# Performance work log

Measured on AMD Instinct MI355X. Metric: run time of the kernel, lower is better.

Reference implementation:

```python
import jax, jax.numpy as jnp
import numpy as np

HEADS = 8
HID = 128
N_A = 10000
N_B = 10000
E = 120000
NG = 8  # graphs in batch
F_A = 256
F_B = 128
NEG_SLOPE = 0.2


def _gat(h_src, h_dst, src, dst, ws, wd, a_s, a_d, bias, num_dst):
    """PyG GATConv, bipartite, concat=False, add_self_loops=False."""
    hs = (h_src @ ws).reshape(-1, HEADS, HID)   # [N_src, H, C]
    hd = (h_dst @ wd).reshape(-1, HEADS, HID)   # [N_dst, H, C]
    al_s = jnp.sum(hs * a_s, axis=-1)           # [N_src, H]
    al_d = jnp.sum(hd * a_d, axis=-1)           # [N_dst, H]
    e = jax.nn.leaky_relu(al_s[src] + al_d[dst], NEG_SLOPE)  # [E, H]
    m = jax.ops.segment_max(e, dst, num_segments=num_dst)
    ex = jnp.exp(e - m[dst])
    denom = jax.ops.segment_sum(ex, dst, num_segments=num_dst)
    alpha = ex / (denom[dst] + 1e-16)           # segment softmax over in-edges
    msg = hs[src] * alpha[:, :, None]           # [E, H, C]
    out = jax.ops.segment_sum(msg, dst, num_segments=num_dst)
    return out.mean(axis=1) + bias              # concat=False -> head mean + bias


def _mean_pool(x, batch, num_graphs):
    s = jax.ops.segment_sum(x, batch, num_segments=num_graphs)
    cnt = jax.ops.segment_sum(jnp.ones((x.shape[0],), x.dtype), batch, num_segments=num_graphs)
    return s / jnp.maximum(cnt, 1.0)[:, None]


def setup_inputs() -> dict:
    key = jax.random.key(0)
    ks = iter(jax.random.split(key, 48))
    rn = lambda shape, s=0.05: jax.random.normal(next(ks), shape, jnp.float32) * s
    inp = {
        'x_a': jax.random.normal(next(ks), (N_A, F_A), jnp.float32),
        'x_b': jax.random.normal(next(ks), (N_B, F_B), jnp.float32),
        'edge_ab': jax.random.randint(next(ks), (2, E), 0, N_A, jnp.int32),
        'edge_ba': jax.random.randint(next(ks), (2, E), 0, N_B, jnp.int32),
        'batch_a': jnp.sort(jax.random.randint(next(ks), (N_A,), 0, NG, jnp.int32)),
        'batch_b': jnp.sort(jax.random.randint(next(ks), (N_B,), 0, NG, jnp.int32)),
        'lin_a_w': rn((F_A, HID)), 'lin_a_b': rn((HID,)),
        'lin_b_w': rn((F_B, HID)), 'lin_b_b': rn((HID,)),
        'fc_w': rn((2 * HID, 1)), 'fc_b': rn((1,)),
    }
    for layer in ('1', '2'):
        for rel in ('ab', 'ba'):
            inp[f'w{layer}s_{rel}'] = rn((HID, HEADS * HID))
            inp[f'w{layer}d_{rel}'] = rn((HID, HEADS * HID))
            inp[f'a{layer}s_{rel}'] = rn((HEADS, HID))
            inp[f'a{layer}d_{rel}'] = rn((HEADS, HID))
            inp[f'b{layer}_{rel}'] = rn((HID,))
    return inp


def reference(x_a, x_b, edge_ab, edge_ba, batch_a, batch_b,
              lin_a_w, lin_a_b, lin_b_w, lin_b_b, fc_w, fc_b,
              w1s_ab, w1d_ab, a1s_ab, a1d_ab, b1_ab,
              w1s_ba, w1d_ba, a1s_ba, a1d_ba, b1_ba,
              w2s_ab, w2d_ab, a2s_ab, a2d_ab, b2_ab,
              w2s_ba, w2d_ba, a2s_ba, a2d_ba, b2_ba):
    ha = jax.nn.relu(x_a @ lin_a_w + lin_a_b)
    hb = jax.nn.relu(x_b @ lin_b_w + lin_b_b)
    # layer 1 (each dst type receives exactly one relation -> HeteroConv mean is identity)
    hb1 = _gat(ha, hb, edge_ab[0], edge_ab[1], w1s_ab, w1d_ab, a1s_ab, a1d_ab, b1_ab, N_B)
    ha1 = _gat(hb, ha, edge_ba[0], edge_ba[1], w1s_ba, w1d_ba, a1s_ba, a1d_ba, b1_ba, N_A)
    ha1 = jax.nn.relu(ha1)
    hb1 = jax.nn.relu(hb1)
    # layer 2
    hb2 = _gat(ha1, hb1, edge_ab[0], edge_ab[1], w2s_ab, w2d_ab, a2s_ab, a2d_ab, b2_ab, N_B)
    ha2 = _gat(hb1, ha1, edge_ba[0], edge_ba[1], w2s_ba, w2d_ba, a2s_ba, a2d_ba, b2_ba, N_A)
    pa = _mean_pool(ha2, batch_a, NG)
    pb = _mean_pool(hb2, batch_b, NG)
    g = jnp.concatenate([pa, pb], axis=1)       # [NG, 2*HID]
    return (g @ fc_w + fc_b).squeeze(-1)        # [NG]
```

## Files before the change

### kernel.cpp

```cpp
#include <hip/hip_runtime.h>
#include <math.h>

#define HID 128
#define HEADS 8

typedef __attribute__((ext_vector_type(8))) short s16x8;
typedef __attribute__((ext_vector_type(4))) float f32x4;

__device__ __forceinline__ unsigned short bf16_rne(float x) {
  unsigned u = __float_as_uint(x);
  unsigned r = u + 0x7FFFu + ((u >> 16) & 1u);
  return (unsigned short)(r >> 16);
}
__device__ __forceinline__ float bf16f(unsigned short h) {
  return __uint_as_float(((unsigned)h) << 16);
}

struct PrepArgs {
  const float* W[8];
  const float* a[8];
  unsigned short* WThi[4];
  unsigned short* WTlo[4];
  float* v[8];
};
struct PrepX {
  const float* lwa; const float* lwb;
  unsigned short *wa_hi, *wa_lo, *wb_hi, *wb_lo;
  int KA, KB, nta, ntb;
};

__global__ __launch_bounds__(256) void prep_hist(
    PrepArgs p, PrepX px,
    const int* __restrict__ dst_ab, const int* __restrict__ dst_ba,
    int* __restrict__ cnt_ab, int* __restrict__ cnt_ba, int E)
{
  __shared__ float tile[64][65];
  const int bid = blockIdx.x;
  const int tid = threadIdx.x;
  const int a = tid >> 2;
  const int cg = (tid & 3) << 4;

  if (bid < 128) {
    const int g = bid >> 5;
    const int rem = bid & 31;
    const int h = rem >> 2;
    const int t = rem & 3;
    const int k0 = (t >> 1) << 6, c0 = (t & 1) << 6;
    const float* src = p.W[2 * g] + (size_t)(k0 + a) * 1024 + h * 128 + c0 + cg;
#pragma unroll
    for (int i = 0; i < 16; i += 4) {
      const float4 v4 = *(const float4*)(src + i);
      tile[a][cg + i + 0] = v4.x; tile[a][cg + i + 1] = v4.y;
      tile[a][cg + i + 2] = v4.z; tile[a][cg + i + 3] = v4.w;
    }
    __syncthreads();
    const size_t ob = (size_t)(c0 + a) * 1024 + h * 128 + k0 + cg;
    unsigned hw[8], lw_[8];
#pragma unroll
    for (int i = 0; i < 8; i++) {
      float x0 = tile[cg + 2 * i][a];
      float x1 = tile[cg + 2 * i + 1][a];
      unsigned short h0 = bf16_rne(x0), h1 = bf16_rne(x1);
      unsigned short l0 = bf16_rne(x0 - bf16f(h0)), l1 = bf16_rne(x1 - bf16f(h1));
      hw[i]  = (unsigned)h0 | ((unsigned)h1 << 16);
      lw_[i] = (unsigned)l0 | ((unsigned)l1 << 16);
    }
    *(uint4*)(p.WThi[g] + ob)     = make_uint4(hw[0], hw[1], hw[2], hw[3]);
    *(uint4*)(p.WThi[g] + ob + 8) = make_uint4(hw[4], hw[5], hw[6], hw[7]);
    *(uint4*)(p.WTlo[g] + ob)     = make_uint4(lw_[0], lw_[1], lw_[2], lw_[3]);
    *(uint4*)(p.WTlo[g] + ob + 8) = make_uint4(lw_[4], lw_[5], lw_[6], lw_[7]);
  } else if (bid < 160) {
    const int u = bid - 128;
    const int wi = u >> 2;
    const int gid = ((u & 3) << 8) + tid;
    const int k = gid >> 3, h = gid & 7;
    const float* wr = p.W[wi] + (size_t)k * (HEADS * HID) + h * HID;
    const float* ar = p.a[wi] + (size_t)h * HID;
    float s = 0.f;
    for (int c = 0; c < HID; c++) s = fmaf(wr[c], ar[c], s);
    p.v[wi][gid] = s;
  } else if (bid < 160 + px.nta + px.ntb) {
    const bool isa = (bid - 160) < px.nta;
    const int b = isa ? (bid - 160) : (bid - 160 - px.nta);
    const int K = isa ? px.KA : px.KB;
    const float* lw = isa ? px.lwa : px.lwb;
    unsigned short* ohi = isa ? px.wa_hi : px.wb_hi;
    unsigned short* olo = isa ? px.wa_lo : px.wb_lo;
    const int k0 = (b >> 1) << 6, c0 = (b & 1) << 6;
    const float* src = lw + (size_t)(k0 + a) * 128 + c0 + cg;
#pragma unroll
    for (int i = 0; i < 16; i += 4) {
      const float4 v4 = *(const float4*)(src + i);
      tile[a][cg + i + 0] = v4.x; tile[a][cg + i + 1] = v4.y;
      tile[a][cg + i + 2] = v4.z; tile[a][cg + i + 3] = v4.w;
    }
    __syncthreads();
    const size_t ob = (size_t)(c0 + a) * K + k0 + cg;
    unsigned hw[8], lw_[8];
#pragma unroll
    for (int i = 0; i < 8; i++) {
      float x0 = tile[cg + 2 * i][a];
      float x1 = tile[cg + 2 * i + 1][a];
      unsigned short h0 = bf16_rne(x0), h1 = bf16_rne(x1);
      unsigned short l0 = bf16_rne(x0 - bf16f(h0)), l1 = bf16_rne(x1 - bf16f(h1));
      hw[i]  = (unsigned)h0 | ((unsigned)h1 << 16);
      lw_[i] = (unsigned)l0 | ((unsigned)l1 << 16);
    }
    *(uint4*)(ohi + ob)     = make_uint4(hw[0], hw[1], hw[2], hw[3]);
    *(uint4*)(ohi + ob + 8) = make_uint4(hw[4], hw[5], hw[6], hw[7]);
    *(uint4*)(olo + ob)     = make_uint4(lw_[0], lw_[1], lw_[2], lw_[3]);
    *(uint4*)(olo + ob + 8) = make_uint4(lw_[4], lw_[5], lw_[6], lw_[7]);
  } else {
    int gid = (bid - 160 - px.nta - px.ntb) * 256 + tid;
    if (gid < E) atomicAdd(&cnt_ab[dst_ab[gid]], 1);
    else if (gid < 2 * E) atomicAdd(&cnt_ba[dst_ba[gid - E]], 1);
  }
}

__global__ __launch_bounds__(1024) void scan2(
    const int* __restrict__ cnt_ab, const int* __restrict__ cnt_ba,
    int* __restrict__ ip_ab, int* __restrict__ ip_ba, int n_ab, int n_ba)
{
  const int* cnt = (blockIdx.x == 0) ? cnt_ab : cnt_ba;
  int* indptr = (blockIdx.x == 0) ? ip_ab : ip_ba;
  int n = (blockIdx.x == 0) ? n_ab : n_ba;
  __shared__ int parts[1024];
  const int tid = threadIdx.x;
  const int base = tid * 10;
  int local[10];
  int s = 0;
#pragma unroll
  for (int j = 0; j < 10; j++) {
    int v = (base + j < n) ? cnt[base + j] : 0;
    local[j] = v; s += v;
  }
  parts[tid] = s;
  __syncthreads();
  for (int off = 1; off < 1024; off <<= 1) {
    int v = (tid >= off) ? parts[tid - off] : 0;
    __syncthreads();
    parts[tid] += v;
    __syncthreads();
  }
  int ex = parts[tid] - s;
#pragma unroll
  for (int j = 0; j < 10; j++) {
    if (base + j < n) indptr[base + j] = ex;
    ex += local[j];
  }
  if (tid == 1023) indptr[n] = parts[1023];
}

__global__ __launch_bounds__(256) void scatter2(
    const int* __restrict__ edge_ab, const int* __restrict__ edge_ba,
    const int* __restrict__ ip_ab, const int* __restrict__ ip_ba,
    int* __restrict__ cur_ab, int* __restrict__ cur_ba,
    int* __restrict__ srcs_ab, int* __restrict__ srcs_ba, int E)
{
  int gid = blockIdx.x * 256 + threadIdx.x;
  if (gid < E) {
    int d = edge_ab[E + gid];
    int pos = ip_ab[d] + atomicAdd(&cur_ab[d], 1);
    srcs_ab[pos] = edge_ab[gid];
  } else if (gid < 2 * E) {
    int g = gid - E;
    int d = edge_ba[E + g];
    int pos = ip_ba[d] + atomicAdd(&cur_ba[d], 1);
    srcs_ba[pos] = edge_ba[g];
  }
}

struct ISeg {
  const float* A;
  const unsigned short* Bhi; const unsigned short* Blo;
  float* out; const float* bias; int M; int K; int yb;
};

__global__ __launch_bounds__(256) void gemm_mfma_in(ISeg s0, ISeg s1)
{
  __shared__ __align__(16) unsigned short smem[12288];
  const int tid = threadIdx.x;
  const float* A; const unsigned short *Bhi, *Blo; const float* bias; float* out;
  int M, K, ytile;
  if ((int)blockIdx.x < s0.yb) {
    A = s0.A; Bhi = s0.Bhi; Blo = s0.Blo; out = s0.out; bias = s0.bias;
    M = s0.M; K = s0.K; ytile = blockIdx.x;
  } else {
    A = s1.A; Bhi = s1.Bhi; Blo = s1.Blo; out = s1.out; bias = s1.bias;
    M = s1.M; K = s1.K; ytile = blockIdx.x - s0.yb;
  }
  const int bm = ytile * 64;
  const int nks = K >> 5;

  const int sr = tid >> 2;
  const int sg = tid & 3;
  const int g1 = sg ^ ((sr >> 1) & 3);
  const int sr2 = sr + 64;
  const int g2 = sg ^ ((sr2 >> 1) & 3);
  const int aslot  = sr * 32 + g1 * 8;
  const int bslotA = sr * 32 + g1 * 8;
  const int bslotB = sr2 * 32 + g2 * 8;
  const int gr = bm + sr;
  const bool arow_ok = (gr < M);
  const float* gA = A + (size_t)gr * K + sg * 8;
  const unsigned short* gB0 = Bhi + (size_t)sr  * K + sg * 8;
  const unsigned short* gB1 = Bhi + (size_t)sr2 * K + sg * 8;
  const unsigned short* gC0 = Blo + (size_t)sr  * K + sg * 8;
  const unsigned short* gC1 = Blo + (size_t)sr2 * K + sg * 8;

  const int l = tid & 63;
  const int w = tid >> 6;
  const int kg = l >> 4;
  int aoff[4], boff[2];
#pragma unroll
  for (int mi = 0; mi < 4; mi++) {
    int r = mi * 16 + (l & 15);
    aoff[mi] = r * 32 + (kg ^ ((r >> 1) & 3)) * 8;
  }
#pragma unroll
  for (int ni = 0; ni < 2; ni++) {
    int r = w * 32 + ni * 16 + (l & 15);
    boff[ni] = r * 32 + (kg ^ ((r >> 1) & 3)) * 8;
  }

  f32x4 acc[4][2];
  const f32x4 z4 = {0.f, 0.f, 0.f, 0.f};
#pragma unroll
  for (int mi = 0; mi < 4; mi++)
#pragma unroll
    for (int ni = 0; ni < 2; ni++) acc[mi][ni] = z4;

  float4 fa0 = make_float4(0.f, 0.f, 0.f, 0.f), fa1 = fa0;
  if (arow_ok) { fa0 = *(const float4*)gA; fa1 = *(const float4*)(gA + 4); }
  uint4 rB0 = *(const uint4*)gB0;
  uint4 rB1 = *(const uint4*)gB1;
  uint4 rC0 = *(const uint4*)gC0;
  uint4 rC1 = *(const uint4*)gC1;

  for (int ks = 0; ks < nks; ks++) {
    {
      const float f[8] = {fa0.x, fa0.y, fa0.z, fa0.w, fa1.x, fa1.y, fa1.z, fa1.w};
      unsigned au[4], lu[4];
#pragma unroll
      for (int i = 0; i < 4; i++) {
        unsigned short h0 = bf16_rne(f[2 * i]);
        unsigned short l0 = bf16_rne(f[2 * i] - bf16f(h0));
        unsigned short h1 = bf16_rne(f[2 * i + 1]);
        unsigned short l1 = bf16_rne(f[2 * i + 1] - bf16f(h1));
        au[i] = (unsigned)h0 | ((unsigned)h1 << 16);
        lu[i] = (unsigned)l0 | ((unsigned)l1 << 16);
      }
      *(uint4*)&smem[aslot]        = make_uint4(au[0], au[1], au[2], au[3]);
      *(uint4*)&smem[2048 + aslot] = make_uint4(lu[0], lu[1], lu[2], lu[3]);
    }
    *(uint4*)&smem[4096 + bslotA] = rB0;
    *(uint4*)&smem[4096 + bslotB] = rB1;
    *(uint4*)&smem[8192 + bslotA] = rC0;
    *(uint4*)&smem[8192 + bslotB] = rC1;
    __syncthreads();
    if (ks < nks - 1) {
      const int k0 = (ks + 1) * 32;
      if (arow_ok) {
        fa0 = *(const float4*)(gA + k0);
        fa1 = *(const float4*)(gA + k0 + 4);
      }
      rB0 = *(const uint4*)(gB0 + k0);
      rB1 = *(const uint4*)(gB1 + k0);
      rC0 = *(const uint4*)(gC0 + k0);
      rC1 = *(const uint4*)(gC1 + k0);
    }
    s16x8 bh0 = *(const s16x8*)&smem[4096 + boff[0]];
    s16x8 bh1 = *(const s16x8*)&smem[4096 + boff[1]];
    s16x8 bl0 = *(const s16x8*)&smem[8192 + boff[0]];
    s16x8 bl1 = *(const s16x8*)&smem[8192 + boff[1]];
#pragma unroll
    for (int mi = 0; mi < 4; mi++) {
      s16x8 ah = *(const s16x8*)&smem[aoff[mi]];
      s16x8 al = *(const s16x8*)&smem[2048 + aoff[mi]];
      acc[mi][0] = __builtin_amdgcn_mfma_f32_16x16x32_bf16(ah, bh0, acc[mi][0], 0, 0, 0);
      acc[mi][1] = __builtin_amdgcn_mfma_f32_16x16x32_bf16(ah, bh1, acc[mi][1], 0, 0, 0);
      acc[mi][0] = __builtin_amdgcn_mfma_f32_16x16x32_bf16(ah, bl0, acc[mi][0], 0, 0, 0);
      acc[mi][1] = __builtin_amdgcn_mfma_f32_16x16x32_bf16(ah, bl1, acc[mi][1], 0, 0, 0);
      acc[mi][0] = __builtin_amdgcn_mfma_f32_16x16x32_bf16(al, bh0, acc[mi][0], 0, 0, 0);
      acc[mi][1] = __builtin_amdgcn_mfma_f32_16x16x32_bf16(al, bh1, acc[mi][1], 0, 0, 0);
      acc[mi][0] = __builtin_amdgcn_mfma_f32_16x16x32_bf16(al, bl0, acc[mi][0], 0, 0, 0);
      acc[mi][1] = __builtin_amdgcn_mfma_f32_16x16x32_bf16(al, bl1, acc[mi][1], 0, 0, 0);
    }
    __syncthreads();
  }

  const int q = l >> 4, cl = l & 15;
#pragma unroll
  for (int ni = 0; ni < 2; ni++) {
    const int col = w * 32 + ni * 16 + cl;
    const float bv = bias[col];
#pragma unroll
    for (int mi = 0; mi < 4; mi++) {
      const int r0 = bm + mi * 16 + q * 4;
      const f32x4 v = acc[mi][ni];
#pragma unroll
      for (int j = 0; j < 4; j++) {
        const int r = r0 + j;
        if (r < M) {
          float x = v[j] + bv;
          x = fmaxf(x, 0.f);
          out[(size_t)r * HID + col] = x;
        }
      }
    }
  }
}

__global__ __launch_bounds__(256) void compute_al4(
    const float* __restrict__ ha, const float* __restrict__ hb,
    const float* __restrict__ v4,
    float* __restrict__ o0, float* __restrict__ o1,
    float* __restrict__ o2, float* __restrict__ o3, int na, int nb)
{
  __shared__ float vsh[4 * HID * HEADS];
  for (int i = threadIdx.x; i < 4 * HID * HEADS; i += 256) vsh[i] = v4[i];
  __syncthreads();
  int gid = blockIdx.x * 256 + threadIdx.x;
  int row = gid >> 3, h = gid & 7;
  const float* hr; float* o; int q, rl;
  if (row < na)                    { q = 0; rl = row;               hr = ha; o = o0; }
  else if (row < na + nb)          { q = 1; rl = row - na;          hr = hb; o = o1; }
  else if (row < na + 2 * nb)      { q = 2; rl = row - na - nb;     hr = hb; o = o2; }
  else if (row < 2 * na + 2 * nb)  { q = 3; rl = row - na - 2 * nb; hr = ha; o = o3; }
  else return;
  hr += (size_t)rl * HID;
  const float* vq = vsh + q * HID * HEADS;
  float s = 0.f;
  for (int k = 0; k < HID; k++) s = fmaf(hr[k], vq[k * HEADS + h], s);
  o[(size_t)rl * HEADS + h] = s;
}

struct GDir {
  const int* indptr; const int* srcs;
  const float* als; const float* ald;
  const float* h;
  unsigned short* zhi; unsigned short* zlo;
};

__global__ __launch_bounds__(256) void gat_edge2(GDir d0, GDir d1, int n0, int ntot)
{
  const int w = threadIdx.x >> 6;
  const int lane = threadIdx.x & 63;
  const int g = blockIdx.x * 4 + w;
  if (g >= ntot) return;
  const bool first = (g < n0);
  const int n = first ? g : g - n0;
  const int* indptr = first ? d0.indptr : d1.indptr;
  const int* srcs   = first ? d0.srcs   : d1.srcs;
  const float* als  = first ? d0.als    : d1.als;
  const float* ald  = first ? d0.ald    : d1.ald;
  const float* hsrc = first ? d0.h      : d1.h;
  unsigned short* zh = (first ? d0.zhi : d1.zhi) + (size_t)n * (HEADS * HID);
  unsigned short* zl = (first ? d0.zlo : d1.zlo) + (size_t)n * (HEADS * HID);

  const int base = indptr[n];
  const int deg = indptr[n + 1] - base;
  if (deg == 0) {
#pragma unroll
    for (int hh = 0; hh < HEADS; hh++) {
      *(unsigned*)(zh + hh * HID + 2 * lane) = 0u;
      *(unsigned*)(zl + hh * HID + 2 * lane) = 0u;
    }
    return;
  }
  const int eh = lane >> 3, h = lane & 7;
  const float aldn = ald[(size_t)n * HEADS + h];
  const int nch = (deg + 7) >> 3;
  const int ncc = nch < 4 ? nch : 4;

  int sc[4];
  float vc[4];
#pragma unroll
  for (int c = 0; c < 4; c++) {
    int e = c * 8 + eh;
    sc[c] = (c < ncc && e < deg) ? srcs[base + e] : -1;
  }
#pragma unroll
  for (int c = 0; c < 4; c++)
    vc[c] = (sc[c] >= 0) ? als[(size_t)sc[c] * HEADS + h] : 0.f;
  float den = 0.f;
#pragma unroll
  for (int c = 0; c < 4; c++) {
    float v = vc[c] + aldn;
    v = v > 0.f ? v : 0.2f * v;
    float ex = (sc[c] >= 0) ? expf(v) : 0.f;
    vc[c] = ex;
    den += ex;
  }
  for (int e0 = 32; e0 < deg; e0 += 8) {
    int e = e0 + eh;
    if (e < deg) {
      int s = srcs[base + e];
      float v = als[(size_t)s * HEADS + h] + aldn;
      v = v > 0.f ? v : 0.2f * v;
      den += expf(v);
    }
  }
  den += __shfl_xor(den, 8);
  den += __shfl_xor(den, 16);
  den += __shfl_xor(den, 32);

  float acc[16];
#pragma unroll
  for (int i = 0; i < 16; i++) acc[i] = 0.f;
#pragma unroll
  for (int c = 0; c < 4; c++) {
    if (c >= ncc) break;
    const int rem = deg - c * 8;
    const int elim = rem < 8 ? rem : 8;
#pragma unroll
    for (int half = 0; half < 2; half++) {
      if (half * 4 >= elim) break;
      int sj[4];
#pragma unroll
      for (int j = 0; j < 4; j++) {
        int s = __shfl(sc[c], (half * 4 + j) * 8);
        sj[j] = s < 0 ? 0 : s;
      }
      float2 hv[4];
#pragma unroll
      for (int j = 0; j < 4; j++)
        hv[j] = *(const float2*)(hsrc + (size_t)sj[j] * HID + 2 * lane);
#pragma unroll
      for (int j = 0; j < 4; j++) {
#pragma unroll
        for (int hh = 0; hh < 8; hh++) {
          float a = __shfl(vc[c], (half * 4 + j) * 8 + hh);
          acc[2 * hh]     = fmaf(a, hv[j].x, acc[2 * hh]);
          acc[2 * hh + 1] = fmaf(a, hv[j].y, acc[2 * hh + 1]);
        }
      }
    }
  }
  for (int e0 = 32; e0 < deg; e0 += 8) {
    int e = e0 + eh;
    int s = (e < deg) ? srcs[base + e] : -1;
    float ex = 0.f;
    if (s >= 0) {
      float v = als[(size_t)s * HEADS + h] + aldn;
      v = v > 0.f ? v : 0.2f * v;
      ex = expf(v);
    }
    int elim = deg - e0; if (elim > 8) elim = 8;
    for (int e8 = 0; e8 < elim; e8++) {
      int ss = __shfl(s, e8 * 8);
      const float2 hvt = *(const float2*)(hsrc + (size_t)ss * HID + 2 * lane);
#pragma unroll
      for (int hh = 0; hh < 8; hh++) {
        float a = __shfl(ex, e8 * 8 + hh);
        acc[2 * hh]     = fmaf(a, hvt.x, acc[2 * hh]);
        acc[2 * hh + 1] = fmaf(a, hvt.y, acc[2 * hh + 1]);
      }
    }
  }
#pragma unroll
  for (int hh = 0; hh < 8; hh++) {
    float dh = __shfl(den, hh);
    float inv = 1.f / (dh + 1e-16f);
    float x0 = acc[2 * hh] * inv;
    float x1 = acc[2 * hh + 1] * inv;
    unsigned short h0 = bf16_rne(x0), h1 = bf16_rne(x1);
    unsigned short l0 = bf16_rne(x0 - bf16f(h0)), l1 = bf16_rne(x1 - bf16f(h1));
    *(unsigned*)(zh + hh * HID + 2 * lane) = (unsigned)h0 | ((unsigned)h1 << 16);
    *(unsigned*)(zl + hh * HID + 2 * lane) = (unsigned)l0 | ((unsigned)l1 << 16);
  }
}

struct MSeg {
  const unsigned short* Ahi; const unsigned short* Alo;
  const unsigned short* Bhi; const unsigned short* Blo;
  int M; int yb;
};

__global__ __launch_bounds__(256, 2) void gemm_mfma_splitk(
    MSeg s0, MSeg s1, float* __restrict__ P, int Mtot, int KS)
{
  __shared__ __align__(16) unsigned short smem[12288];
  const int tid = threadIdx.x;
  const unsigned short *Ahi, *Alo, *Bhi, *Blo; int M, ytile, rowbase;
  if ((int)blockIdx.x < s0.yb) {
    Ahi = s0.Ahi; Alo = s0.Alo; Bhi = s0.Bhi; Blo = s0.Blo;
    M = s0.M; ytile = blockIdx.x; rowbase = 0;
  } else {
    Ahi = s1.Ahi; Alo = s1.Alo; Bhi = s1.Bhi; Blo = s1.Blo;
    M = s1.M; ytile = blockIdx.x - s0.yb; rowbase = s0.yb * 64;
  }
  const int bm = ytile * 64;
  const int kchunk = 1024 / KS;
  const int kbeg = blockIdx.y * kchunk;
  const int nks = kchunk / 32;

  const int sr = tid >> 2;
  const int sg = tid & 3;
  const int g1 = sg ^ ((sr >> 1) & 3);
  const int sr2 = sr + 64;
  const int g2 = sg ^ ((sr2 >> 1) & 3);
  const int aslot  = sr * 32 + g1 * 8;
  const int bslotA = sr * 32 + g1 * 8;
  const int bslotB = sr2 * 32 + g2 * 8;
  const unsigned short* gA  = Ahi + (size_t)(bm + sr) * 1024 + kbeg + sg * 8;
  const unsigned short* gAl = Alo + (size_t)(bm + sr) * 1024 + kbeg + sg * 8;
  const unsigned short* gB0 = Bhi + (size_t)sr  * 1024 + kbeg + sg * 8;
  const unsigned short* gB1 = Bhi + (size_t)sr2 * 1024 + kbeg + sg * 8;
  const unsigned short* gC0 = Blo + (size_t)sr  * 1024 + kbeg + sg * 8;
  const unsigned short* gC1 = Blo + (size_t)sr2 * 1024 + kbeg + sg * 8;

  const int l = tid & 63;
  const int w = tid >> 6;
  const int kg = l >> 4;
  int aoff[4], boff[2];
#pragma unroll
  for (int mi = 0; mi < 4; mi++) {
    int r = mi * 16 + (l & 15);
    aoff[mi] = r * 32 + (kg ^ ((r >> 1) & 3)) * 8;
  }
#pragma unroll
  for (int ni = 0; ni < 2; ni++) {
    int r = w * 32 + ni * 16 + (l & 15);
    boff[ni] = r * 32 + (kg ^ ((r >> 1) & 3)) * 8;
  }

  f32x4 acc[4][2];
  const f32x4 z4 = {0.f, 0.f, 0.f, 0.f};
#pragma unroll
  for (int mi = 0; mi < 4; mi++)
#pragma unroll
    for (int ni = 0; ni < 2; ni++) acc[mi][ni] = z4;

  uint4 rA  = *(const uint4*)gA;
  uint4 rAl = *(const uint4*)gAl;
  uint4 rB0 = *(const uint4*)gB0;
  uint4 rB1 = *(const uint4*)gB1;
  uint4 rC0 = *(const uint4*)gC0;
  uint4 rC1 = *(const uint4*)gC1;

  for (int ks = 0; ks < nks; ks++) {
    *(uint4*)&smem[aslot]         = rA;
    *(uint4*)&smem[2048 + aslot]  = rAl;
    *(uint4*)&smem[4096 + bslotA] = rB0;
    *(uint4*)&smem[4096 + bslotB] = rB1;
    *(uint4*)&smem[8192 + bslotA] = rC0;
    *(uint4*)&smem[8192 + bslotB] = rC1;
    __syncthreads();
    if (ks < nks - 1) {
      const int k0 = (ks + 1) * 32;
      rA  = *(const uint4*)(gA  + k0);
      rAl = *(const uint4*)(gAl + k0);
      rB0 = *(const uint4*)(gB0 + k0);
      rB1 = *(const uint4*)(gB1 + k0);
      rC0 = *(const uint4*)(gC0 + k0);
      rC1 = *(const uint4*)(gC1 + k0);
    }
    s16x8 bh0 = *(const s16x8*)&smem[4096 + boff[0]];
    s16x8 bh1 = *(const s16x8*)&smem[4096 + boff[1]];
    s16x8 bl0 = *(const s16x8*)&smem[8192 + boff[0]];
    s16x8 bl1 = *(const s16x8*)&smem[8192 + boff[1]];
#pragma unroll
    for (int mi = 0; mi < 4; mi++) {
      s16x8 ah = *(const s16x8*)&smem[aoff[mi]];
      s16x8 al = *(const s16x8*)&smem[2048 + aoff[mi]];
      acc[mi][0] = __builtin_amdgcn_mfma_f32_16x16x32_bf16(ah, bh0, acc[mi][0], 0, 0, 0);
      acc[mi][1] = __builtin_amdgcn_mfma_f32_16x16x32_bf16(ah, bh1, acc[mi][1], 0, 0, 0);
      acc[mi][0] = __builtin_amdgcn_mfma_f32_16x16x32_bf16(ah, bl0, acc[mi][0], 0, 0, 0);
      acc[mi][1] = __builtin_amdgcn_mfma_f32_16x16x32_bf16(ah, bl1, acc[mi][1], 0, 0, 0);
      acc[mi][0] = __builtin_amdgcn_mfma_f32_16x16x32_bf16(al, bh0, acc[mi][0], 0, 0, 0);
      acc[mi][1] = __builtin_amdgcn_mfma_f32_16x16x32_bf16(al, bh1, acc[mi][1], 0, 0, 0);
      acc[mi][0] = __builtin_amdgcn_mfma_f32_16x16x32_bf16(al, bl0, acc[mi][0], 0, 0, 0);
      acc[mi][1] = __builtin_amdgcn_mfma_f32_16x16x32_bf16(al, bl1, acc[mi][1], 0, 0, 0);
    }
    __syncthreads();
  }

  const int q = l >> 4, cl = l & 15;
  const size_t prow0 = (size_t)blockIdx.y * Mtot + rowbase + bm;
#pragma unroll
  for (int ni = 0; ni < 2; ni++) {
    const int col = w * 32 + ni * 16 + cl;
#pragma unroll
    for (int mi = 0; mi < 4; mi++) {
      const int r0 = mi * 16 + q * 4;
      const f32x4 v = acc[mi][ni];
#pragma unroll
      for (int j = 0; j < 4; j++) {
        const int r = r0 + j;
        if (bm + r < M) P[(prow0 + r) * HID + col] = v[j];
      }
    }
  }
}

struct RSegA {
  float* out; const float* bias; int M; int rowbase;
  const float* va; const float* vb;
  float* ala; float* alb;
};

__global__ __launch_bounds__(256) void reduce_epi_al(
    const float* __restrict__ P, int Mtot, int KS, float scale, int do_relu,
    RSegA s0, RSegA s1)
{
  int idx = blockIdx.x * 256 + threadIdx.x;
  if (idx >= Mtot * 32) return;
  int r = idx >> 5;
  int c = (idx & 31) << 2;
  float* outp; const float* bias; int rl;
  const float* va; const float* vb; float* ala; float* alb;
  if (s1.M > 0 && r >= s1.rowbase) {
    rl = r - s1.rowbase; if (rl >= s1.M) return;
    outp = s1.out; bias = s1.bias; va = s1.va; vb = s1.vb; ala = s1.ala; alb = s1.alb;
  } else {
    rl = r; if (rl >= s0.M) return;
    outp = s0.out; bias = s0.bias; va = s0.va; vb = s0.vb; ala = s0.ala; alb = s0.alb;
  }
  float4 acc = make_float4(0.f, 0.f, 0.f, 0.f);
  for (int z = 0; z < KS; z++) {
    const float4 v = *(const float4*)(P + ((size_t)z * Mtot + r) * HID + c);
    acc.x += v.x; acc.y += v.y; acc.z += v.z; acc.w += v.w;
  }
  const float4 b = *(const float4*)(bias + c);
  acc.x = acc.x * scale + b.x;
  acc.y = acc.y * scale + b.y;
  acc.z = acc.z * scale + b.z;
  acc.w = acc.w * scale + b.w;
  if (do_relu) {
    acc.x = fmaxf(acc.x, 0.f); acc.y = fmaxf(acc.y, 0.f);
    acc.z = fmaxf(acc.z, 0.f); acc.w = fmaxf(acc.w, 0.f);
  }
  *(float4*)(outp + (size_t)rl * HID + c) = acc;

  const float av[4] = {acc.x, acc.y, acc.z, acc.w};
  float pA[8], pB[8];
#pragma unroll
  for (int i = 0; i < 8; i++) { pA[i] = 0.f; pB[i] = 0.f; }
#pragma unroll
  for (int j = 0; j < 4; j++) {
    const float4 a0 = *(const float4*)(va + (c + j) * 8);
    const float4 a1 = *(const float4*)(va + (c + j) * 8 + 4);
    const float4 b0 = *(const float4*)(vb + (c + j) * 8);
    const float4 b1 = *(const float4*)(vb + (c + j) * 8 + 4);
    pA[0] = fmaf(av[j], a0.x, pA[0]); pA[1] = fmaf(av[j], a0.y, pA[1]);
    pA[2] = fmaf(av[j], a0.z, pA[2]); pA[3] = fmaf(av[j], a0.w, pA[3]);
    pA[4] = fmaf(av[j], a1.x, pA[4]); pA[5] = fmaf(av[j], a1.y, pA[5]);
    pA[6] = fmaf(av[j], a1.z, pA[6]); pA[7] = fmaf(av[j], a1.w, pA[7]);
    pB[0] = fmaf(av[j], b0.x, pB[0]); pB[1] = fmaf(av[j], b0.y, pB[1]);
    pB[2] = fmaf(av[j], b0.z, pB[2]); pB[3] = fmaf(av[j], b0.w, pB[3]);
    pB[4] = fmaf(av[j], b1.x, pB[4]); pB[5] = fmaf(av[j], b1.y, pB[5]);
    pB[6] = fmaf(av[j], b1.z, pB[6]); pB[7] = fmaf(av[j], b1.w, pB[7]);
  }
#pragma unroll
  for (int off = 16; off >= 1; off >>= 1) {
#pragma unroll
    for (int i = 0; i < 8; i++) {
      pA[i] += __shfl_xor(pA[i], off);
      pB[i] += __shfl_xor(pB[i], off);
    }
  }
  if ((threadIdx.x & 31) == 0) {
    *(float4*)(ala + (size_t)rl * 8)     = make_float4(pA[0], pA[1], pA[2], pA[3]);
    *(float4*)(ala + (size_t)rl * 8 + 4) = make_float4(pA[4], pA[5], pA[6], pA[7]);
    *(float4*)(alb + (size_t)rl * 8)     = make_float4(pB[0], pB[1], pB[2], pB[3]);
    *(float4*)(alb + (size_t)rl * 8 + 4) = make_float4(pB[4], pB[5], pB[6], pB[7]);
  }
}

struct RSeg { float* out; const float* bias; int M; int rowbase; };

__global__ __launch_bounds__(256) void reduce_epi(
    const float* __restrict__ P, int Mtot, int KS, float scale, int do_relu,
    RSeg s0, RSeg s1)
{
  int idx = blockIdx.x * 256 + threadIdx.x;
  if (idx >= Mtot * 32) return;
  int r = idx >> 5;
  int c = (idx & 31) << 2;
  float* outp; const float* bias; int rl;
  if (s1.M > 0 && r >= s1.rowbase) {
    rl = r - s1.rowbase; if (rl >= s1.M) return; outp = s1.out; bias = s1.bias;
  } else {
    rl = r; if (rl >= s0.M) return; outp = s0.out; bias = s0.bias;
  }
  float4 acc = make_float4(0.f, 0.f, 0.f, 0.f);
  for (int z = 0; z < KS; z++) {
    const float4 v = *(const float4*)(P + ((size_t)z * Mtot + r) * HID + c);
    acc.x += v.x; acc.y += v.y; acc.z += v.z; acc.w += v.w;
  }
  const float4 b = *(const float4*)(bias + c);
  acc.x = acc.x * scale + b.x;
  acc.y = acc.y * scale + b.y;
  acc.z = acc.z * scale + b.z;
  acc.w = acc.w * scale + b.w;
  if (do_relu) {
    acc.x = fmaxf(acc.x, 0.f); acc.y = fmaxf(acc.y, 0.f);
    acc.z = fmaxf(acc.z, 0.f); acc.w = fmaxf(acc.w, 0.f);
  }
  *(float4*)(outp + (size_t)rl * HID + c) = acc;
}

__global__ __launch_bounds__(256) void pool_fin(
    const float* __restrict__ ha, const float* __restrict__ hb,
    const int* __restrict__ batch_a, const int* __restrict__ batch_b,
    const float* __restrict__ fc_w, const float* __restrict__ fc_b,
    float* __restrict__ gsum, int* __restrict__ ticket,
    float* __restrict__ out, int na, int nb, int ng)
{
  const bool isA = blockIdx.x < 160;
  const float* h = isA ? ha : hb;
  const int* batch = isA ? batch_a : batch_b;
  const float* wseg = isA ? fc_w : fc_w + HID;
  float* gs = isA ? gsum : gsum + 8;
  const int n = isA ? na : nb;
  const int b = isA ? blockIdx.x : blockIdx.x - 160;

  __shared__ float sg[8];
  __shared__ int lastf;
  if (threadIdx.x < 8) sg[threadIdx.x] = 0.f;
  __syncthreads();
  const int lane = threadIdx.x & 63;
  const int wv = threadIdx.x >> 6;
  const int gw = b * 4 + wv;
  const int tw = 160 * 4;
  const float2 w2 = *(const float2*)(wseg + lane * 2);
  for (int r = gw; r < n; r += tw) {
    float2 hv = *(const float2*)(h + (size_t)r * HID + lane * 2);
    float s = hv.x * w2.x + hv.y * w2.y;
#pragma unroll
    for (int off = 32; off > 0; off >>= 1) s += __shfl_down(s, off, 64);
    if (lane == 0) atomicAdd(&sg[batch[r]], s);
  }
  __syncthreads();
  if (threadIdx.x < 8) atomicAdd(&gs[threadIdx.x], sg[threadIdx.x]);
  if (threadIdx.x == 0) {
    __threadfence();
    int tk = atomicAdd(ticket, 1);
    lastf = (tk == (int)gridDim.x - 1);
  }
  __syncthreads();
  if (lastf) {
    int g = threadIdx.x;
    if (g < ng) {
      int l, r, lo;
      l = 0; r = na; while (l < r) { int m = (l + r) >> 1; if (batch_a[m] < g) l = m + 1; else r = m; } lo = l;
      r = na; while (l < r) { int m = (l + r) >> 1; if (batch_a[m] < g + 1) l = m + 1; else r = m; }
      int ca = l - lo; if (ca < 1) ca = 1;
      l = 0; r = nb; while (l < r) { int m = (l + r) >> 1; if (batch_b[m] < g) l = m + 1; else r = m; } lo = l;
      r = nb; while (l < r) { int m = (l + r) >> 1; if (batch_b[m] < g + 1) l = m + 1; else r = m; }
      int cb = l - lo; if (cb < 1) cb = 1;
      float va = atomicAdd(&gsum[g], 0.f);
      float vb = atomicAdd(&gsum[8 + g], 0.f);
      out[g] = va / (float)ca + vb / (float)cb + fc_b[0];
    }
  }
}

extern "C" void kernel_launch(void* const* d_in, const int* in_sizes, int n_in,
                              void* d_out, int out_size, void* d_ws, size_t ws_size,
                              hipStream_t stream)
{
  const float* x_a = (const float*)d_in[0];
  const float* x_b = (const float*)d_in[1];
  const int* edge_ab = (const int*)d_in[2];
  const int* edge_ba = (const int*)d_in[3];
  const int* batch_a = (const int*)d_in[4];
  const int* batch_b = (const int*)d_in[5];
  const float* lin_a_w = (const float*)d_in[6];
  const float* lin_a_b = (const float*)d_in[7];
  const float* lin_b_w = (const float*)d_in[8];
  const float* lin_b_b = (const float*)d_in[9];
  const float* fc_w = (const float*)d_in[10];
  const float* fc_b = (const float*)d_in[11];

  const int NA = in_sizes[4];
  const int NB = in_sizes[5];
  const int E  = in_sizes[2] / 2;
  const int FA = in_sizes[0] / NA;
  const int FB = in_sizes[1] / NB;
  const int NG = out_size;
  const int NMAX = NA > NB ? NA : NB;
  const int NAp = (NA + 127) & ~127, NBp = (NB + 127) & ~127;
  const int NMAXp = NAp > NBp ? NAp : NBp;
  const int Mtot = NAp + NBp;

  auto al256 = [](size_t b) { return (b + 255) & ~(size_t)255; };
  size_t fixed = 0;
  fixed += 3 * al256((size_t)NAp * HID * 4) + 3 * al256((size_t)NBp * HID * 4);
  fixed += 2 * al256((size_t)NMAXp * 1024 * 2);
  fixed += al256((size_t)8 * 131072 * 2);
  fixed += 2 * al256((size_t)FA * HID * 2) + 2 * al256((size_t)FB * HID * 2);
  fixed += al256((size_t)8 * HID * HEADS * 4);
  fixed += 2 * al256((size_t)NAp * HEADS * 4) + 2 * al256((size_t)NBp * HEADS * 4);
  fixed += al256(((size_t)4 * NMAX + 24) * 4);
  fixed += al256((size_t)(NB + 1) * 4) + al256((size_t)(NA + 1) * 4);
  fixed += 2 * al256((size_t)E * 4);
  fixed += 8192;
  const size_t zba_sz = 2 * al256((size_t)NAp * 1024 * 2);
  const size_t pslice = al256((size_t)Mtot * HID * 4);

  int KS = 4; bool dual = true;
  if (fixed + zba_sz + 4 * pslice <= ws_size)      { dual = true;  KS = 4; }
  else if (fixed + zba_sz + 2 * pslice <= ws_size) { dual = true;  KS = 2; }
  else if (fixed + 4 * pslice <= ws_size)          { dual = false; KS = 4; }
  else if (fixed + 2 * pslice <= ws_size)          { dual = false; KS = 2; }
  else if (fixed + 1 * pslice <= ws_size)          { dual = false; KS = 1; }
  else return;

  char* w = (char*)d_ws;
  auto carve = [&](size_t bytes) -> void* {
    void* p = (void*)w;
    w += (bytes + 255) & ~(size_t)255;
    return p;
  };
  float* ha0 = (float*)carve((size_t)NAp * HID * 4);
  float* hb0 = (float*)carve((size_t)NBp * HID * 4);
  float* ha1 = (float*)carve((size_t)NAp * HID * 4);
  float* hb1 = (float*)carve((size_t)NBp * HID * 4);
  float* ha2 = (float*)carve((size_t)NAp * HID * 4);
  float* hb2 = (float*)carve((size_t)NBp * HID * 4);
  unsigned short* zab_hi = (unsigned short*)carve((size_t)NMAXp * 1024 * 2);
  unsigned short* zab_lo = (unsigned short*)carve((size_t)NMAXp * 1024 * 2);
  unsigned short* zba_hi = dual ? (unsigned short*)carve((size_t)NAp * 1024 * 2) : zab_hi;
  unsigned short* zba_lo = dual ? (unsigned short*)carve((size_t)NAp * 1024 * 2) : zab_lo;
  float* P = (float*)carve((size_t)KS * Mtot * HID * 4);
  unsigned short* WT = (unsigned short*)carve((size_t)8 * 131072 * 2);
  unsigned short* wa_hi = (unsigned short*)carve((size_t)FA * HID * 2);
  unsigned short* wa_lo = (unsigned short*)carve((size_t)FA * HID * 2);
  unsigned short* wb_hi = (unsigned short*)carve((size_t)FB * HID * 2);
  unsigned short* wb_lo = (unsigned short*)carve((size_t)FB * HID * 2);
  float* vv  = (float*)carve((size_t)8 * HID * HEADS * 4);
  float* als_ab = (float*)carve((size_t)NAp * HEADS * 4);
  float* ald_ab = (float*)carve((size_t)NBp * HEADS * 4);
  float* als_ba = (float*)carve((size_t)NBp * HEADS * 4);
  float* ald_ba = (float*)carve((size_t)NAp * HEADS * 4);
  int* csrblk = (int*)carve(((size_t)4 * NMAX + 24) * 4);
  int* indptr_ab = (int*)carve((size_t)(NB + 1) * 4);
  int* indptr_ba = (int*)carve((size_t)(NA + 1) * 4);
  int* srcs_ab   = (int*)carve((size_t)E * 4);
  int* srcs_ba   = (int*)carve((size_t)E * 4);
  if ((size_t)(w - (char*)d_ws) > ws_size) return;

  int* cnt_ab = csrblk;
  int* cnt_ba = csrblk + NMAX;
  int* cur_ab = csrblk + 2 * NMAX;
  int* cur_ba = csrblk + 3 * NMAX;
  float* gsum = (float*)(csrblk + 4 * NMAX);
  int* ticket = csrblk + 4 * NMAX + 16;

  hipMemsetAsync(csrblk, 0, ((size_t)4 * NMAX + 24) * 4, stream);

  PrepArgs pa;
  const int wi_idx[8] = {12, 13, 17, 18, 22, 23, 27, 28};
  const int ai_idx[8] = {14, 15, 19, 20, 24, 25, 29, 30};
  for (int i = 0; i < 8; i++) {
    pa.W[i] = (const float*)d_in[wi_idx[i]];
    pa.a[i] = (const float*)d_in[ai_idx[i]];
    pa.v[i] = vv + (size_t)i * HID * HEADS;
  }
  for (int g = 0; g < 4; g++) {
    pa.WThi[g] = WT + (size_t)g * 131072;
    pa.WTlo[g] = WT + (size_t)(4 + g) * 131072;
  }
  PrepX px;
  px.lwa = lin_a_w; px.lwb = lin_b_w;
  px.wa_hi = wa_hi; px.wa_lo = wa_lo; px.wb_hi = wb_hi; px.wb_lo = wb_lo;
  px.KA = FA; px.KB = FB;
  px.nta = (FA / 64) * 2;
  px.ntb = (FB / 64) * 2;
  const int hist_b = (2 * E + 255) / 256;
  prep_hist<<<160 + px.nta + px.ntb + hist_b, 256, 0, stream>>>(
      pa, px, edge_ab + E, edge_ba + E, cnt_ab, cnt_ba, E);
  scan2<<<2, 1024, 0, stream>>>(cnt_ab, cnt_ba, indptr_ab, indptr_ba, NB, NA);
  scatter2<<<(2 * E + 255) / 256, 256, 0, stream>>>(
      edge_ab, edge_ba, indptr_ab, indptr_ba, cur_ab, cur_ba, srcs_ab, srcs_ba, E);

  {
    ISeg sa = {x_a, wa_hi, wa_lo, ha0, lin_a_b, NA, FA, NAp / 64};
    ISeg sb = {x_b, wb_hi, wb_lo, hb0, lin_b_b, NB, FB, NBp / 64};
    gemm_mfma_in<<<NAp / 64 + NBp / 64, 256, 0, stream>>>(sa, sb);
  }

  const int red_grid = (Mtot * 32 + 255) / 256;

  compute_al4<<<((2 * (NA + NB)) * HEADS + 255) / 256, 256, 0, stream>>>(
      ha0, hb0, vv, als_ab, ald_ab, als_ba, ald_ba, NA, NB);

  GDir dab0 = {indptr_ab, srcs_ab, als_ab, ald_ab, ha0, zab_hi, zab_lo};
  GDir dba0 = {indptr_ba, srcs_ba, als_ba, ald_ba, hb0, zba_hi, zba_lo};
  MSeg mab0 = {zab_hi, zab_lo, WT + (size_t)0 * 131072, WT + (size_t)4 * 131072, NB, NBp / 64};
  MSeg mba0 = {zba_hi, zba_lo, WT + (size_t)1 * 131072, WT + (size_t)5 * 131072, NA, NAp / 64};
  const float* v1 = vv + (size_t)4 * HID * HEADS;

  GDir dab1 = {indptr_ab, srcs_ab, als_ab, ald_ab, ha1, zab_hi, zab_lo};
  GDir dba1 = {indptr_ba, srcs_ba, als_ba, ald_ba, hb1, zba_hi, zba_lo};
  MSeg mab1 = {zab_hi, zab_lo, WT + (size_t)2 * 131072, WT + (size_t)6 * 131072, NB, NBp / 64};
  MSeg mba1 = {zba_hi, zba_lo, WT + (size_t)3 * 131072, WT + (size_t)7 * 131072, NA, NAp / 64};

  if (dual) {
    gat_edge2<<<(NB + NA + 3) / 4, 256, 0, stream>>>(dab0, dba0, NB, NB + NA);
    gemm_mfma_splitk<<<dim3(NBp / 64 + NAp / 64, KS), 256, 0, stream>>>(mab0, mba0, P, Mtot, KS);
    RSegA r0 = {hb1, (const float*)d_in[16], NB, 0,
                v1 + 1024, v1 + 2048, ald_ab, als_ba};
    RSegA r1 = {ha1, (const float*)d_in[21], NA, NBp,
                v1, v1 + 3072, als_ab, ald_ba};
    reduce_epi_al<<<red_grid, 256, 0, stream>>>(P, Mtot, KS, 1.f / HEADS, 1, r0, r1);
    gat_edge2<<<(NB + NA + 3) / 4, 256, 0, stream>>>(dab1, dba1, NB, NB + NA);
    gemm_mfma_splitk<<<dim3(NBp / 64 + NAp / 64, KS), 256, 0, stream>>>(mab1, mba1, P, Mtot, KS);
    RSeg p0 = {hb2, (const float*)d_in[26], NB, 0};
    RSeg p1 = {ha2, (const float*)d_in[31], NA, NBp};
    reduce_epi<<<red_grid, 256, 0, stream>>>(P, Mtot, KS, 1.f / HEADS, 0, p0, p1);
  } else {
    const RSegA ranull = {nullptr, nullptr, 0, 0, nullptr, nullptr, nullptr, nullptr};
    const RSeg rnull = {nullptr, nullptr, 0, 0};
    gat_edge2<<<(NB + 3) / 4, 256, 0, stream>>>(dab0, dab0, NB, NB);
    {
      MSeg mz = {nullptr, nullptr, nullptr, nullptr, 0, 0};
      gemm_mfma_splitk<<<dim3(NBp / 64, KS), 256, 0, stream>>>(mab0, mz, P, NBp, KS);
      RSegA r0 = {hb1, (const float*)d_in[16], NB, 0, v1 + 1024, v1 + 2048, ald_ab, als_ba};
      reduce_epi_al<<<(NBp * 32 + 255) / 256, 256, 0, stream>>>(P, NBp, KS, 1.f / HEADS, 1, r0, ranull);
    }
    gat_edge2<<<(NA + 3) / 4, 256, 0, stream>>>(dba0, dba0, NA, NA);
    {
      MSeg mz = {nullptr, nullptr, nullptr, nullptr, 0, 0};
      gemm_mfma_splitk<<<dim3(NAp / 64, KS), 256, 0, stream>>>(mba0, mz, P, NAp, KS);
      RSegA r1 = {ha1, (const float*)d_in[21], NA, 0, v1, v1 + 3072, als_ab, ald_ba};
      reduce_epi_al<<<(NAp * 32 + 255) / 256, 256, 0, stream>>>(P, NAp, KS, 1.f / HEADS, 1, r1, ranull);
    }
    gat_edge2<<<(NB + 3) / 4, 256, 0, stream>>>(dab1, dab1, NB, NB);
    {
      MSeg mz = {nullptr, nullptr, nullptr, nullptr, 0, 0};
      gemm_mfma_splitk<<<dim3(NBp / 64, KS), 256, 0, stream>>>(mab1, mz, P, NBp, KS);
      RSeg p0 = {hb2, (const float*)d_in[26], NB, 0};
      reduce_epi<<<(NBp * 32 + 255) / 256, 256, 0, stream>>>(P, NBp, KS, 1.f / HEADS, 0, p0, rnull);
    }
    gat_edge2<<<(NA + 3) / 4, 256, 0, stream>>>(dba1, dba1, NA, NA);
    {
      MSeg mz = {nullptr, nullptr, nullptr, nullptr, 0, 0};
      gemm_mfma_splitk<<<dim3(NAp / 64, KS), 256, 0, stream>>>(mba1, mz, P, NAp, KS);
      RSeg p1 = {ha2, (const float*)d_in[31], NA, 0};
      reduce_epi<<<(NAp * 32 + 255) / 256, 256, 0, stream>>>(P, NAp, KS, 1.f / HEADS, 0, p1, rnull);
    }
  }

  pool_fin<<<320, 256, 0, stream>>>(ha2, hb2, batch_a, batch_b, fc_w, fc_b,
                                    gsum, ticket, (float*)d_out, NA, NB, NG);
}
```

Before: 382.4 us.

## Fuse edge scatter and attention-logit computation into input-projection GEMM kernel

Merges the CSR scatter kernel into the input GEMM launch as extra blocks, and computes the per-node attention logits in the GEMM epilogue from an LDS-staged tile of the relu output instead of running a separate compute_al4 kernel. This removes two launches and a re-read of ha0/hb0 from global memory. In exchange the GEMM kernel uses more shared memory (an extra 64x133 float tile), which may lower occupancy. The epilogue dot products run on only 64 threads per block reading attention vectors from global memory.

```diff
diff --git a/kernel.cpp b/kernel.cpp
--- a/kernel.cpp
+++ b/kernel.cpp
@@ -151,43 +151,51 @@
   if (tid == 1023) indptr[n] = parts[1023];
 }
 
-__global__ __launch_bounds__(256) void scatter2(
-    const int* __restrict__ edge_ab, const int* __restrict__ edge_ba,
-    const int* __restrict__ ip_ab, const int* __restrict__ ip_ba,
-    int* __restrict__ cur_ab, int* __restrict__ cur_ba,
-    int* __restrict__ srcs_ab, int* __restrict__ srcs_ba, int E)
-{
-  int gid = blockIdx.x * 256 + threadIdx.x;
-  if (gid < E) {
-    int d = edge_ab[E + gid];
-    int pos = ip_ab[d] + atomicAdd(&cur_ab[d], 1);
-    srcs_ab[pos] = edge_ab[gid];
-  } else if (gid < 2 * E) {
-    int g = gid - E;
-    int d = edge_ba[E + g];
-    int pos = ip_ba[d] + atomicAdd(&cur_ba[d], 1);
-    srcs_ba[pos] = edge_ba[g];
-  }
-}
-
 struct ISeg {
   const float* A;
   const unsigned short* Bhi; const unsigned short* Blo;
   float* out; const float* bias; int M; int K; int yb;
+  const float* va; const float* vb;
+  float* ala; float* alb;
 };
 
-__global__ __launch_bounds__(256) void gemm_mfma_in(ISeg s0, ISeg s1)
+__global__ __launch_bounds__(256) void gemm_in_fused(
+    const int* __restrict__ edge_ab, const int* __restrict__ edge_ba,
+    const int* __restrict__ ip_ab, const int* __restrict__ ip_ba,
+    int* __restrict__ cur_ab, int* __restrict__ cur_ba,
+    int* __restrict__ srcs_ab, int* __restrict__ srcs_ba, int E, int scat_b,
+    ISeg s0, ISeg s1)
 {
   __shared__ __align__(16) unsigned short smem[12288];
+  __shared__ float fl[64][133];
   const int tid = threadIdx.x;
+  const int bid0 = blockIdx.x;
+  if (bid0 < scat_b) {
+    int gid = bid0 * 256 + tid;
+    if (gid < E) {
+      int d = edge_ab[E + gid];
+      int pos = ip_ab[d] + atomicAdd(&cur_ab[d], 1);
+      srcs_ab[pos] = edge_ab[gid];
+    } else if (gid < 2 * E) {
+      int g = gid - E;
+      int d = edge_ba[E + g];
+      int pos = ip_ba[d] + atomicAdd(&cur_ba[d], 1);
+      srcs_ba[pos] = edge_ba[g];
+    }
+    return;
+  }
+  const int gemm_bid = bid0 - scat_b;
   const float* A; const unsigned short *Bhi, *Blo; const float* bias; float* out;
+  const float* va; const float* vb; float* ala; float* alb;
   int M, K, ytile;
-  if ((int)blockIdx.x < s0.yb) {
+  if (gemm_bid < s0.yb) {
     A = s0.A; Bhi = s0.Bhi; Blo = s0.Blo; out = s0.out; bias = s0.bias;
-    M = s0.M; K = s0.K; ytile = blockIdx.x;
+    M = s0.M; K = s0.K; ytile = gemm_bid;
+    va = s0.va; vb = s0.vb; ala = s0.ala; alb = s0.alb;
   } else {
     A = s1.A; Bhi = s1.Bhi; Blo = s1.Blo; out = s1.out; bias = s1.bias;
-    M = s1.M; K = s1.K; ytile = blockIdx.x - s0.yb;
+    M = s1.M; K = s1.K; ytile = gemm_bid - s0.yb;
+    va = s1.va; vb = s1.vb; ala = s1.ala; alb = s1.alb;
   }
   const int bm = ytile * 64;
   const int nks = K >> 5;
@@ -296,43 +304,48 @@
     const float bv = bias[col];
 #pragma unroll
     for (int mi = 0; mi < 4; mi++) {
-      const int r0 = bm + mi * 16 + q * 4;
+      const int rt = mi * 16 + q * 4;
       const f32x4 v = acc[mi][ni];
 #pragma unroll
       for (int j = 0; j < 4; j++) {
-        const int r = r0 + j;
+        const int r = bm + rt + j;
         if (r < M) {
           float x = v[j] + bv;
           x = fmaxf(x, 0.f);
           out[(size_t)r * HID + col] = x;
+          fl[rt + j][col] = x;
         }
       }
     }
   }
-}
-
-__global__ __launch_bounds__(256) void compute_al4(
-    const float* __restrict__ ha, const float* __restrict__ hb,
-    const float* __restrict__ v4,
-    float* __restrict__ o0, float* __restrict__ o1,
-    float* __restrict__ o2, float* __restrict__ o3, int na, int nb)
-{
-  __shared__ float vsh[4 * HID * HEADS];
-  for (int i = threadIdx.x; i < 4 * HID * HEADS; i += 256) vsh[i] = v4[i];
   __syncthreads();
-  int gid = blockIdx.x * 256 + threadIdx.x;
-  int row = gid >> 3, h = gid & 7;
-  const float* hr; float* o; int q, rl;
-  if (row < na)                    { q = 0; rl = row;               hr = ha; o = o0; }
-  else if (row < na + nb)          { q = 1; rl = row - na;          hr = hb; o = o1; }
-  else if (row < na + 2 * nb)      { q = 2; rl = row - na - nb;     hr = hb; o = o2; }
-  else if (row < 2 * na + 2 * nb)  { q = 3; rl = row - na - 2 * nb; hr = ha; o = o3; }
-  else return;
-  hr += (size_t)rl * HID;
-  const float* vq = vsh + q * HID * HEADS;
-  float s = 0.f;
-  for (int k = 0; k < HID; k++) s = fmaf(hr[k], vq[k * HEADS + h], s);
-  o[(size_t)rl * HEADS + h] = s;
+  if (tid < 64) {
+    const int r = bm + tid;
+    if (r < M) {
+      float pA[8], pB[8];
+#pragma unroll
+      for (int i = 0; i < 8; i++) { pA[i] = 0.f; pB[i] = 0.f; }
+      for (int col = 0; col < HID; col++) {
+        const float hv = fl[tid][col];
+        const float4 a0 = *(const float4*)(va + col * 8);
+        const float4 a1 = *(const float4*)(va + col * 8 + 4);
+        const float4 b0 = *(const float4*)(vb + col * 8);
+        const float4 b1 = *(const float4*)(vb + col * 8 + 4);
+        pA[0] = fmaf(hv, a0.x, pA[0]); pA[1] = fmaf(hv, a0.y, pA[1]);
+        pA[2] = fmaf(hv, a0.z, pA[2]); pA[3] = fmaf(hv, a0.w, pA[3]);
+        pA[4] = fmaf(hv, a1.x, pA[4]); pA[5] = fmaf(hv, a1.y, pA[5]);
+        pA[6] = fmaf(hv, a1.z, pA[6]); pA[7] = fmaf(hv, a1.w, pA[7]);
+        pB[0] = fmaf(hv, b0.x, pB[0]); pB[1] = fmaf(hv, b0.y, pB[1]);
+        pB[2] = fmaf(hv, b0.z, pB[2]); pB[3] = fmaf(hv, b0.w, pB[3]);
+        pB[4] = fmaf(hv, b1.x, pB[4]); pB[5] = fmaf(hv, b1.y, pB[5]);
+        pB[6] = fmaf(hv, b1.z, pB[6]); pB[7] = fmaf(hv, b1.w, pB[7]);
+      }
+      *(float4*)(ala + (size_t)r * 8)     = make_float4(pA[0], pA[1], pA[2], pA[3]);
+      *(float4*)(ala + (size_t)r * 8 + 4) = make_float4(pA[4], pA[5], pA[6], pA[7]);
+      *(float4*)(alb + (size_t)r * 8)     = make_float4(pB[0], pB[1], pB[2], pB[3]);
+      *(float4*)(alb + (size_t)r * 8 + 4) = make_float4(pB[4], pB[5], pB[6], pB[7]);
+    }
+  }
 }
 
 struct GDir {
@@ -873,19 +886,19 @@
   prep_hist<<<160 + px.nta + px.ntb + hist_b, 256, 0, stream>>>(
       pa, px, edge_ab + E, edge_ba + E, cnt_ab, cnt_ba, E);
   scan2<<<2, 1024, 0, stream>>>(cnt_ab, cnt_ba, indptr_ab, indptr_ba, NB, NA);
-  scatter2<<<(2 * E + 255) / 256, 256, 0, stream>>>(
-      edge_ab, edge_ba, indptr_ab, indptr_ba, cur_ab, cur_ba, srcs_ab, srcs_ba, E);
 
   {
-    ISeg sa = {x_a, wa_hi, wa_lo, ha0, lin_a_b, NA, FA, NAp / 64};
-    ISeg sb = {x_b, wb_hi, wb_lo, hb0, lin_b_b, NB, FB, NBp / 64};
-    gemm_mfma_in<<<NAp / 64 + NBp / 64, 256, 0, stream>>>(sa, sb);
+    ISeg sa = {x_a, wa_hi, wa_lo, ha0, lin_a_b, NA, FA, NAp / 64,
+               vv + 0 * 1024, vv + 3 * 1024, als_ab, ald_ba};
+    ISeg sb = {x_b, wb_hi, wb_lo, hb0, lin_b_b, NB, FB, NBp / 64,
+               vv + 1 * 1024, vv + 2 * 1024, ald_ab, als_ba};
+    const int scat_b = (2 * E + 255) / 256;
+    gemm_in_fused<<<scat_b + NAp / 64 + NBp / 64, 256, 0, stream>>>(
+        edge_ab, edge_ba, indptr_ab, indptr_ba, cur_ab, cur_ba,
+        srcs_ab, srcs_ba, E, scat_b, sa, sb);
   }
 
   const int red_grid = (Mtot * 32 + 255) / 256;
-
-  compute_al4<<<((2 * (NA + NB)) * HEADS + 255) / 256, 256, 0, stream>>>(
-      ha0, hb0, vv, als_ab, ald_ab, als_ba, ald_ba, NA, NB);
 
   GDir dab0 = {indptr_ab, srcs_ab, als_ab, ald_ab, ha0, zab_hi, zab_lo};
   GDir dba0 = {indptr_ba, srcs_ba, als_ba, ald_ba, hb0, zba_hi, zba_lo};
```

Measured after the change: 381.9 us. No clear change (-0.1%).
